# Optimization experiments

Measured on AMD Instinct MI355X. Metric: run time of the kernel, lower is better.

The kernel has to match this reference:

```python
import jax, jax.numpy as jnp
import numpy as np
from jax.scipy.linalg import solve_triangular

N, K, D = 131072, 8, 32  # samples, clusters, dims


def setup_inputs() -> dict:
    key = jax.random.key(0)
    k1, k2, k3, k4 = jax.random.split(key, 4)
    return {
        "X": jax.random.normal(k1, (N, D), dtype=jnp.float32),
        "mu": jax.random.normal(k2, (K, D), dtype=jnp.float32),
        "L": jax.random.normal(k3, (K, D, D), dtype=jnp.float32),
        "weights": jax.random.normal(k4, (K,), dtype=jnp.float32),
        "it": 0,
    }


def _mixture_log_likelihoods(X, mu, L, weights):
    K_, D_ = mu.shape
    LOG2PI = float(np.log(2.0 * np.pi))
    # update_covariances: A_k = L_k L_k^T + I  (always SPD -> cholesky succeeds)
    A = jnp.einsum('kab,kcb->kac', L, L) + jnp.eye(D_, dtype=L.dtype)
    Lc = jnp.linalg.cholesky(A)            # [K,D,D] lower Cholesky factors
    invLc = jnp.linalg.inv(Lc)             # [K,D,D]
    # all cluster pairs (cartesian_prod order: i outer, j inner)
    ii, jj = [g.reshape(-1) for g in jnp.meshgrid(jnp.arange(K_), jnp.arange(K_), indexing='ij')]
    Si, Sj = Lc[ii], Lc[jj]                # NOTE: original uses the CHOLESKY FACTORS here
    invSi, invSj = invLc[ii], invLc[jj]
    mui, muj = mu[ii], mu[jj]
    # _gaussian_product: sigma = inv(inv(Si)+inv(Sj)); mu = sigma @ (inv(Si) mu_i + inv(Sj) mu_j)
    sigma = jnp.linalg.inv(invSi + invSj)                      # [P,D,D]
    rhs = jnp.einsum('pab,pb->pa', invSi, mui) + jnp.einsum('pab,pb->pa', invSj, muj)
    mu_p = jnp.einsum('pab,pb->pa', sigma, rhs)                # [P,D]
    # _product_z: log(1/sqrt(det(2*pi*(Si+Sj))) * exp(-0.5 dmu^T inv(Si+Sj) dmu))
    S = Si + Sj
    dmu = mui - muj
    quad = -0.5 * jnp.einsum('pa,pab,pb->p', dmu, jnp.linalg.inv(S), dmu)
    z = -0.5 * jnp.log(jnp.linalg.det(2.0 * np.pi * S)) + quad  # [P]
    # _unormalised_pdf: lower-triangular solve against sigma (only lower triangle used)
    diff = X[None, :, :] - mu_p[:, None, :]                    # [P,N,D]
    m = solve_triangular(sigma, jnp.swapaxes(diff, 1, 2), lower=True)  # [P,D,N]
    ll = -0.5 * (jnp.sum(m * m, axis=1) + D_ * LOG2PI
                 + jnp.log(jnp.linalg.det(sigma))[:, None])    # [P,N]
    logw = jax.nn.log_softmax(weights)                         # softmax weights, then log
    logprob = z[:, None] + ll + logw[ii][:, None] + logw[jj][:, None]  # [P,N]
    return jnp.log(jnp.sum(jnp.exp(logprob), axis=0))          # [N]


def reference(X, mu, L, weights, it):
    ll = _mixture_log_likelihoods(X, mu, L, weights)
    return jax.scipy.special.logsumexp(ll, axis=0)  # scalar
```

## Files before the change

### kernel.cpp

```cpp
#include <hip/hip_runtime.h>

#define D 32
#define K 8
#define NPAIR 36
#define PROWS 576

#define PMOFF 0
#define WOFF 4608
#define C2OFF 4864
#define CMAXOFF 4900
#define LCOFF 4928
#define PARTOFF 13120

typedef float v2f __attribute__((ext_vector_type(2)));

__host__ __device__ constexpr int gidx(int i, int j) {
    return i * 8 + j - i * (i + 1) / 2;
}
__host__ __device__ constexpr int proff(int r) {
    return 4 * (r / 4 + 1) * (2 * (r / 4) + (r % 4));
}

__global__ __launch_bounds__(64) void setup1_kernel(
    const float* __restrict__ mu, const float* __restrict__ L,
    float* __restrict__ ws)
{
    __shared__ float sA[D][D + 1];
    __shared__ float sLc[D][D + 1];
    __shared__ float sI[D][D + 1];
    const int k = blockIdx.x;
    const int tid = threadIdx.x;
    const int i = tid & 31;

    for (int e = tid; e < D * D; e += 64) sI[e >> 5][e & 31] = L[k * D * D + e];
    __syncthreads();

    for (int e = tid; e < D * D; e += 64) {
        const int a = e >> 5, c = e & 31;
        float s = (a == c) ? 1.0f : 0.0f;
        #pragma unroll
        for (int b = 0; b < D; ++b) s = fmaf(sI[a][b], sI[c][b], s);
        sA[a][c] = s;
    }
    __syncthreads();

    float lrow[D];
    #pragma unroll
    for (int j = 0; j < D; ++j) {
        if (i == j) {
            float s = sA[j][j];
            #pragma unroll
            for (int b = 0; b < j; ++b) s = fmaf(-lrow[b], lrow[b], s);
            const float d = sqrtf(s);
            lrow[j] = d;
            #pragma unroll
            for (int b = 0; b < j; ++b) sLc[j][b] = lrow[b];
            sLc[j][j] = d;
        }
        __syncthreads();
        if (i > j) {
            float s = sA[i][j];
            #pragma unroll
            for (int b = 0; b < j; ++b) s = fmaf(-lrow[b], sLc[j][b], s);
            lrow[j] = s / sLc[j][j];
        }
    }
    __syncthreads();

    for (int e = tid; e < D * D; e += 64) {
        const int r = e >> 5, c = e & 31;
        ws[LCOFF + k * D * D + e] = (c <= r) ? sLc[r][c] : 0.0f;
    }

    {
        const int j = i;
        #pragma unroll
        for (int ii = 0; ii < D; ++ii) {
            float s = (ii == j) ? 1.0f : 0.0f;
            #pragma unroll
            for (int b = 0; b < ii; ++b) s = fmaf(-sLc[ii][b], sI[b][j], s);
            const float cii = s / sLc[ii][ii];
            sI[ii][j] = cii;
            const int w4 = 4 * (ii / 4 + 1);
            if (j < w4) ws[PMOFF + k * PROWS + proff(ii) + j] = cii;
        }
    }
    __syncthreads();

    {
        float s = 0.0f;
        #pragma unroll
        for (int b = 0; b < D; ++b) s = fmaf(sI[i][b], mu[k * D + b], s);
        ws[WOFF + k * D + i] = s;
    }
}

#define SLC(kk, r, c) sLc2[(kk) * 1024 + (r) * 32 + (c)]

__global__ __launch_bounds__(256) void setup2_kernel(
    const float* __restrict__ mu, const float* __restrict__ weights,
    float* __restrict__ ws)
{
    __shared__ float sLc2[K * D * D];
    __shared__ float sMu[K * D];
    __shared__ float sWt[K];
    __shared__ float sLogw[K];
    __shared__ float sCp[NPAIR];
    __shared__ float sCmax;
    const int tid = threadIdx.x;

    {
        const float4* src = (const float4*)(ws + LCOFF);
        float4* dst = (float4*)sLc2;
        #pragma unroll
        for (int e = 0; e < 8; ++e) dst[tid + 256 * e] = src[tid + 256 * e];
        sMu[tid] = mu[tid];
        if (tid < K) sWt[tid] = weights[tid];
    }
    __syncthreads();

    if (tid == 0) {
        float m = -INFINITY;
        for (int t = 0; t < K; ++t) m = fmaxf(m, sWt[t]);
        float s = 0.0f;
        for (int t = 0; t < K; ++t) s += expf(sWt[t] - m);
        const float lse = m + logf(s);
        for (int t = 0; t < K; ++t) sLogw[t] = sWt[t] - lse;
    }
    __syncthreads();

    if (tid < NPAIR) {
        int tt = tid, pi = 0;
        while (tt >= (K - pi)) { tt -= (K - pi); ++pi; }
        const int pj = pi + tt;
        const float LOG2PI = 1.8378770664093453f;
        float sumlogS = 0.0f, logdetsig = 0.0f;
        #pragma unroll
        for (int r = 0; r < D; ++r) {
            const float di = SLC(pi, r, r), dj = SLC(pj, r, r);
            sumlogS += logf(di + dj);
            logdetsig -= logf(1.0f / di + 1.0f / dj);
        }
        float v[D];
        float quad_acc = 0.0f;
        #pragma unroll
        for (int r = 0; r < D; ++r) {
            const float d0 = sMu[pi * D + r] - sMu[pj * D + r];
            float s = d0;
            #pragma unroll
            for (int b = 0; b < r; ++b)
                s = fmaf(-(SLC(pi, r, b) + SLC(pj, r, b)), v[b], s);
            v[r] = s / (SLC(pi, r, r) + SLC(pj, r, r));
            quad_acc = fmaf(d0, v[r], quad_acc);
        }
        const float quad = -0.5f * quad_acc;
        float c = quad - 0.5f * sumlogS - (float)D * LOG2PI - 0.5f * logdetsig
                  + sLogw[pi] + sLogw[pj];
        if (pi < pj) c += 0.6931471805599453f;
        sCp[tid] = c;
    }
    __syncthreads();
    if (tid == 0) {
        float m = -INFINITY;
        for (int t = 0; t < NPAIR; ++t) m = fmaxf(m, sCp[t]);
        sCmax = m;
        ws[CMAXOFF] = m;
    }
    __syncthreads();
    if (tid < NPAIR)
        ws[C2OFF + tid] = (sCp[tid] - sCmax) * 1.4426950408889634f;
}

#define XCHG 4864

__global__ __launch_bounds__(128, 2) void main_kernel(
    const float* __restrict__ X, const float* __restrict__ cst,
    float* __restrict__ partials, int nsamp)
{
    __shared__ __align__(16) float sBig[XCHG];
    __shared__ __align__(16) float sW[K * D];
    __shared__ float sC2[NPAIR];
    const int tid = threadIdx.x;
    const int wv = tid >> 6;
    const int lane = tid & 63;

    const int n0 = blockIdx.x * 128 + lane;
    const int n1 = n0 + 64;
    const int m0 = (n0 < nsamp) ? n0 : 0;
    const int m1 = (n1 < nsamp) ? n1 : 0;

    v2f xa[16], xb[16];
    {
        const float4* Xv0 = (const float4*)(X + m0 * D);
        const float4* Xv1 = (const float4*)(X + m1 * D);
        #pragma unroll
        for (int q = 0; q < 8; ++q) {
            const float4 t0 = Xv0[q];
            xa[2 * q]     = (v2f){t0.x, t0.y};
            xa[2 * q + 1] = (v2f){t0.z, t0.w};
            const float4 t1 = Xv1[q];
            xb[2 * q]     = (v2f){t1.x, t1.y};
            xb[2 * q + 1] = (v2f){t1.z, t1.w};
        }
    }

    {
        const float4* src = (const float4*)cst;
        float4* dst = (float4*)sBig;
        for (int e = tid; e < K * PROWS / 4; e += 128) dst[e] = src[e];
        const float4* srcw = (const float4*)(cst + WOFF);
        float4* dstw = (float4*)sW;
        if (tid < K * D / 4) dstw[tid] = srcw[tid];
        if (tid < NPAIR) sC2[tid] = cst[C2OFF + tid];
    }
    __syncthreads();

    v2f G2[NPAIR];
    #pragma unroll
    for (int t = 0; t < NPAIR; ++t) G2[t] = (v2f){0.0f, 0.0f};

    #pragma unroll
    for (int rh = 0; rh < 8; ++rh) {
        if ((rh & 1) == wv) {
            #pragma unroll
            for (int rr = 0; rr < 4; ++rr) {
                const int r = 4 * rh + rr;
                v2f ya[K], yb[K];
                #pragma unroll
                for (int k = 0; k < K; ++k) {
                    const float wvv = sW[k * D + r];
                    v2f a0 = (v2f){-wvv, 0.0f};
                    v2f a1 = (v2f){-wvv, 0.0f};
                    const float* Mr = sBig + k * PROWS + proff(r);
                    #pragma unroll
                    for (int c4 = 0; c4 <= rh; ++c4) {
                        const float4 m4 = *(const float4*)(Mr + 4 * c4);
                        const v2f mlo = (v2f){m4.x, m4.y};
                        const v2f mhi = (v2f){m4.z, m4.w};
                        a0 = __builtin_elementwise_fma(mlo, xa[2 * c4],     a0);
                        a1 = __builtin_elementwise_fma(mlo, xb[2 * c4],     a1);
                        a0 = __builtin_elementwise_fma(mhi, xa[2 * c4 + 1], a0);
                        a1 = __builtin_elementwise_fma(mhi, xb[2 * c4 + 1], a1);
                    }
                    ya[k] = a0;  yb[k] = a1;
                }
                v2f y2[K];
                #pragma unroll
                for (int k = 0; k < K; ++k)
                    y2[k] = (v2f){ya[k].x + ya[k].y, yb[k].x + yb[k].y};
                #pragma unroll
                for (int pi = 0; pi < K; ++pi)
                    #pragma unroll
                    for (int pj = pi; pj < K; ++pj)
                        G2[gidx(pi, pj)] = __builtin_elementwise_fma(
                            y2[pi], y2[pj], G2[gidx(pi, pj)]);
            }
        }
    }

    __syncthreads();

    if (wv == 1) {
        float2* xch = (float2*)sBig;
        #pragma unroll
        for (int t = 0; t < NPAIR; ++t)
            xch[t * 65 + lane] = make_float2(G2[t].x, G2[t].y);
    }
    __syncthreads();

    if (wv == 0) {
        const float2* xch = (const float2*)sBig;
        #pragma unroll
        for (int t = 0; t < NPAIR; ++t) {
            const float2 g = xch[t * 65 + lane];
            G2[t] += (v2f){g.x, g.y};
        }

        v2f acc2 = (v2f){0.0f, 0.0f};
        const float NH = -0.72134752044448170f;
        #pragma unroll
        for (int pi = 0; pi < K; ++pi)
            #pragma unroll
            for (int pj = pi; pj < K; ++pj) {
                const v2f q2 = __builtin_elementwise_fma(
                    (v2f){2.0f, 2.0f}, G2[gidx(pi, pj)],
                    G2[gidx(pi, pi)] + G2[gidx(pj, pj)]);
                const float c = sC2[gidx(pi, pj)];
                const v2f e2 = __builtin_elementwise_fma((v2f){NH, NH}, q2,
                                                         (v2f){c, c});
                acc2.x += exp2f(e2.x);
                acc2.y += exp2f(e2.y);
            }
        float acc = ((n0 < nsamp) ? acc2.x : 0.0f)
                  + ((n1 < nsamp) ? acc2.y : 0.0f);

        #pragma unroll
        for (int s = 1; s < 64; s <<= 1) acc += __shfl_xor(acc, s, 64);
        if (lane == 0) partials[blockIdx.x] = acc;
    }
}

__global__ __launch_bounds__(256) void finish_kernel(
    const float* __restrict__ partials, const float* __restrict__ ws,
    float* __restrict__ out, int nblk)
{
    __shared__ float sRed[4];
    const int tid = threadIdx.x;
    float acc = 0.0f;
    for (int e = tid; e < nblk; e += 256) acc += partials[e];
    #pragma unroll
    for (int s = 1; s < 64; s <<= 1) acc += __shfl_xor(acc, s, 64);
    if ((tid & 63) == 0) sRed[tid >> 6] = acc;
    __syncthreads();
    if (tid == 0) out[0] = ws[CMAXOFF] + logf(sRed[0] + sRed[1] + sRed[2] + sRed[3]);
}

extern "C" void kernel_launch(void* const* d_in, const int* in_sizes, int n_in,
                              void* d_out, int out_size, void* d_ws, size_t ws_size,
                              hipStream_t stream) {
    const float* X = (const float*)d_in[0];
    const float* mu = (const float*)d_in[1];
    const float* L = (const float*)d_in[2];
    const float* w = (const float*)d_in[3];
    float* wsf = (float*)d_ws;
    float* out = (float*)d_out;

    const int nsamp = in_sizes[0] / D;
    const int nblk = (nsamp + 127) / 128;

    setup1_kernel<<<K, 64, 0, stream>>>(mu, L, wsf);
    setup2_kernel<<<1, 256, 0, stream>>>(mu, w, wsf);
    main_kernel<<<nblk, 128, 0, stream>>>(X, wsf, wsf + PARTOFF, nsamp);
    finish_kernel<<<1, 256, 0, stream>>>(wsf + PARTOFF, wsf, out, nblk);
}
```

Baseline: 139.6 us.

## Split triangular row work across four waves with balanced pairing and tree reduction

The main kernel now launches 256 threads per block. All four waves work on the same 128 samples, and each wave takes two row-blocks of the triangular solve, rh and 7-rh, so the triangular work is balanced across waves. The per-pair Gram accumulators are combined through a two-level LDS exchange that uses a second shared buffer. This adds parallelism per sample and is meant to shorten the per-thread dependency chain. The costs are redundant X loads in every wave, extra barriers, more LDS, and possible register pressure under the tighter launch bounds.

```diff
diff --git a/kernel.cpp b/kernel.cpp
--- a/kernel.cpp
+++ b/kernel.cpp
@@ -171,13 +171,12 @@
         ws[C2OFF + tid] = (sCp[tid] - sCmax) * 1.4426950408889634f;
 }
 
-#define XCHG 4864
-
-__global__ __launch_bounds__(128, 2) void main_kernel(
+__global__ __launch_bounds__(256, 4) void main_kernel(
     const float* __restrict__ X, const float* __restrict__ cst,
     float* __restrict__ partials, int nsamp)
 {
-    __shared__ __align__(16) float sBig[XCHG];
+    __shared__ __align__(16) float sBig[K * PROWS];
+    __shared__ __align__(16) float sX1[K * PROWS];
     __shared__ __align__(16) float sW[K * D];
     __shared__ float sC2[NPAIR];
     const int tid = threadIdx.x;
@@ -207,7 +206,7 @@
     {
         const float4* src = (const float4*)cst;
         float4* dst = (float4*)sBig;
-        for (int e = tid; e < K * PROWS / 4; e += 128) dst[e] = src[e];
+        for (int e = tid; e < K * PROWS / 4; e += 256) dst[e] = src[e];
         const float4* srcw = (const float4*)(cst + WOFF);
         float4* dstw = (float4*)sW;
         if (tid < K * D / 4) dstw[tid] = srcw[tid];
@@ -221,7 +220,7 @@
 
     #pragma unroll
     for (int rh = 0; rh < 8; ++rh) {
-        if ((rh & 1) == wv) {
+        if (rh == wv || rh == 7 - wv) {
             #pragma unroll
             for (int rr = 0; rr < 4; ++rr) {
                 const int r = 4 * rh + rr;
@@ -260,19 +259,43 @@
 
     __syncthreads();
 
+    float2* xchA = (float2*)sBig;
+    float2* xchB = (float2*)sX1;
     if (wv == 1) {
-        float2* xch = (float2*)sBig;
         #pragma unroll
         for (int t = 0; t < NPAIR; ++t)
-            xch[t * 65 + lane] = make_float2(G2[t].x, G2[t].y);
-    }
-    __syncthreads();
-
+            xchA[t * 64 + lane] = make_float2(G2[t].x, G2[t].y);
+    } else if (wv == 3) {
+        #pragma unroll
+        for (int t = 0; t < NPAIR; ++t)
+            xchB[t * 64 + lane] = make_float2(G2[t].x, G2[t].y);
+    }
+    __syncthreads();
     if (wv == 0) {
-        const float2* xch = (const float2*)sBig;
         #pragma unroll
         for (int t = 0; t < NPAIR; ++t) {
-            const float2 g = xch[t * 65 + lane];
+            const float2 g = xchA[t * 64 + lane];
+            G2[t] += (v2f){g.x, g.y};
+        }
+    } else if (wv == 2) {
+        #pragma unroll
+        for (int t = 0; t < NPAIR; ++t) {
+            const float2 g = xchB[t * 64 + lane];
+            G2[t] += (v2f){g.x, g.y};
+        }
+    }
+    __syncthreads();
+    if (wv == 2) {
+        #pragma unroll
+        for (int t = 0; t < NPAIR; ++t)
+            xchA[t * 64 + lane] = make_float2(G2[t].x, G2[t].y);
+    }
+    __syncthreads();
+
+    if (wv == 0) {
+        #pragma unroll
+        for (int t = 0; t < NPAIR; ++t) {
+            const float2 g = xchA[t * 64 + lane];
             G2[t] += (v2f){g.x, g.y};
         }
 
@@ -330,6 +353,6 @@
 
     setup1_kernel<<<K, 64, 0, stream>>>(mu, L, wsf);
     setup2_kernel<<<1, 256, 0, stream>>>(mu, w, wsf);
-    main_kernel<<<nblk, 128, 0, stream>>>(X, wsf, wsf + PARTOFF, nsamp);
+    main_kernel<<<nblk, 256, 0, stream>>>(X, wsf, wsf + PARTOFF, nsamp);
     finish_kernel<<<1, 256, 0, stream>>>(wsf + PARTOFF, wsf, out, nblk);
 }
```

After: 361.2 us. 159% more time.

## Fuse final reduction into main kernel via atomics and rebalance row halves

Applied to the files above, without the earlier changes.

Removes the separate finish kernel: each block atomically adds its partial sum to a global accumulator, and the last block to increment a counter computes the final log. The accumulator and counter are zeroed in setup2. The triangular row blocks are also reassigned across the two waves with an XOR pattern so each wave gets a more balanced share of the work. The goal is to drop one kernel launch and balance per-wave work, at the cost of atomic contention across 1024 blocks and a nondeterministic float summation order.

```diff
diff --git a/kernel.cpp b/kernel.cpp
--- a/kernel.cpp
+++ b/kernel.cpp
@@ -9,8 +9,9 @@
 #define WOFF 4608
 #define C2OFF 4864
 #define CMAXOFF 4900
+#define ACCOFF 4904
+#define CNTOFF 4908
 #define LCOFF 4928
-#define PARTOFF 13120
 
 typedef float v2f __attribute__((ext_vector_type(2)));
 
@@ -117,6 +118,10 @@
         sMu[tid] = mu[tid];
         if (tid < K) sWt[tid] = weights[tid];
     }
+    if (tid == 0) {
+        ws[ACCOFF] = 0.0f;
+        *((int*)(ws + CNTOFF)) = 0;
+    }
     __syncthreads();
 
     if (tid == 0) {
@@ -174,8 +179,8 @@
 #define XCHG 4864
 
 __global__ __launch_bounds__(128, 2) void main_kernel(
-    const float* __restrict__ X, const float* __restrict__ cst,
-    float* __restrict__ partials, int nsamp)
+    const float* __restrict__ X, float* __restrict__ cst,
+    float* __restrict__ out, int nsamp, int nblk)
 {
     __shared__ __align__(16) float sBig[XCHG];
     __shared__ __align__(16) float sW[K * D];
@@ -221,7 +226,7 @@
 
     #pragma unroll
     for (int rh = 0; rh < 8; ++rh) {
-        if ((rh & 1) == wv) {
+        if ((((rh >> 1) ^ rh) & 1) == wv) {
             #pragma unroll
             for (int rr = 0; rr < 4; ++rr) {
                 const int r = 4 * rh + rr;
@@ -296,23 +301,18 @@
 
         #pragma unroll
         for (int s = 1; s < 64; s <<= 1) acc += __shfl_xor(acc, s, 64);
-        if (lane == 0) partials[blockIdx.x] = acc;
-    }
-}
-
-__global__ __launch_bounds__(256) void finish_kernel(
-    const float* __restrict__ partials, const float* __restrict__ ws,
-    float* __restrict__ out, int nblk)
-{
-    __shared__ float sRed[4];
-    const int tid = threadIdx.x;
-    float acc = 0.0f;
-    for (int e = tid; e < nblk; e += 256) acc += partials[e];
-    #pragma unroll
-    for (int s = 1; s < 64; s <<= 1) acc += __shfl_xor(acc, s, 64);
-    if ((tid & 63) == 0) sRed[tid >> 6] = acc;
-    __syncthreads();
-    if (tid == 0) out[0] = ws[CMAXOFF] + logf(sRed[0] + sRed[1] + sRed[2] + sRed[3]);
+
+        if (lane == 0) {
+            atomicAdd(cst + ACCOFF, acc);
+            __threadfence();
+            const int old = atomicAdd((int*)(cst + CNTOFF), 1);
+            if (old == nblk - 1) {
+                __threadfence();
+                const float total = atomicAdd(cst + ACCOFF, 0.0f);
+                out[0] = cst[CMAXOFF] + logf(total);
+            }
+        }
+    }
 }
 
 extern "C" void kernel_launch(void* const* d_in, const int* in_sizes, int n_in,
@@ -330,6 +330,5 @@
 
     setup1_kernel<<<K, 64, 0, stream>>>(mu, L, wsf);
     setup2_kernel<<<1, 256, 0, stream>>>(mu, w, wsf);
-    main_kernel<<<nblk, 128, 0, stream>>>(X, wsf, wsf + PARTOFF, nsamp);
-    finish_kernel<<<1, 256, 0, stream>>>(wsf + PARTOFF, wsf, out, nblk);
-}
+    main_kernel<<<nblk, 128, 0, stream>>>(X, wsf, out, nsamp, nblk);
+}
```

After: 158.2 us. 1.13x slower.
